# Kernel optimization log

Measured on AMD Instinct MI355X. Metric: run time of the kernel, lower is better.

## Reference

```python
import jax, jax.numpy as jnp
import numpy as np

B, C, T = 128, 23, 2000
N_FFT, HOP = 200, 100
NFREQ = N_FFT // 2 + 1        # 101
FT = 1 + (T - N_FFT) // HOP   # 19 time frames per channel
EMB, HEADS, DEPTH = 256, 8, 4
DH = EMB // HEADS             # 32 head dim
FF = 4 * EMB                  # 1024 ffn hidden
MASK_RATIO = 0.15


def _posenc(n, d):
    pos = np.arange(n)[:, None].astype(np.float32)
    div = np.exp(np.arange(0, d, 2).astype(np.float32) * -(np.log(10000.0) / d))
    pe = np.zeros((n, d), np.float32)
    pe[:, 0::2] = np.sin(pos * div)
    pe[:, 1::2] = np.cos(pos * div)
    return jnp.asarray(pe)


def _stft_mag(sig):
    # sig: (..., T) -> (..., FT, NFREQ); rectangular window, center=False, onesided
    idx = np.arange(FT)[:, None] * HOP + np.arange(N_FFT)[None, :]
    frames = sig[..., idx]                      # (..., FT, N_FFT)
    return jnp.abs(jnp.fft.rfft(frames, axis=-1))


def _layernorm(x, g, b):
    mu = x.mean(-1, keepdims=True)
    var = x.var(-1, keepdims=True)
    return (x - mu) / jnp.sqrt(var + 1e-5) * g + b


def setup_inputs() -> dict:
    key = jax.random.key(0)
    ks = jax.random.split(key, 12)
    inp = {
        'x': jax.random.normal(ks[0], (B, C, T), jnp.float32),
        'mask': jax.random.uniform(ks[1], (B, C, T)) < MASK_RATIO,
        'n_channel_offset': 0,
        'W_proj': jax.random.normal(ks[2], (NFREQ, EMB), jnp.float32) / np.sqrt(NFREQ),
        'b_proj': jnp.zeros((EMB,), jnp.float32),
        'channel_tokens': jax.random.normal(ks[3], (C, EMB), jnp.float32),
        'ln1_g': jnp.ones((DEPTH, EMB), jnp.float32),
        'ln1_b': jnp.zeros((DEPTH, EMB), jnp.float32),
        'Wq': jax.random.normal(ks[4], (DEPTH, EMB, EMB), jnp.float32) / np.sqrt(EMB),
        'Wk': jax.random.normal(ks[5], (DEPTH, EMB, EMB), jnp.float32) / np.sqrt(EMB),
        'Wv': jax.random.normal(ks[6], (DEPTH, EMB, EMB), jnp.float32) / np.sqrt(EMB),
        'Wo': jax.random.normal(ks[7], (DEPTH, EMB, EMB), jnp.float32) / np.sqrt(EMB),
        'ln2_g': jnp.ones((DEPTH, EMB), jnp.float32),
        'ln2_b': jnp.zeros((DEPTH, EMB), jnp.float32),
        'W1': jax.random.normal(ks[8], (DEPTH, EMB, FF), jnp.float32) / np.sqrt(EMB),
        'b1': jnp.zeros((DEPTH, FF), jnp.float32),
        'W2': jax.random.normal(ks[9], (DEPTH, FF, EMB), jnp.float32) / np.sqrt(FF),
        'b2': jnp.zeros((DEPTH, EMB), jnp.float32),
    }
    return inp


def reference(x, mask, n_channel_offset, W_proj, b_proj, channel_tokens,
              ln1_g, ln1_b, Wq, Wk, Wv, Wo, ln2_g, ln2_b, W1, b1, W2, b2):
    xm = jnp.where(mask, 0.0, x)
    # STFT magnitude for all channels at once: (B, C, FT, NFREQ)
    spec_c = _stft_mag(x)
    spec_m = _stft_mag(xm)
    # patch-frequency linear embedding -> (B, C, FT, EMB)
    emb_c = spec_c @ W_proj + b_proj
    emb_m = spec_m @ W_proj + b_proj
    tok = jnp.take(channel_tokens, jnp.arange(C) + n_channel_offset, axis=0)
    pe = _posenc(FT, EMB)
    emb_c = emb_c + tok[None, :, None, :] + pe[None, None, :, :]
    emb_m = emb_m + tok[None, :, None, :] + pe[None, None, :, :]
    S = C * FT
    emb_c = emb_c.reshape(B, S, EMB)
    h = emb_m.reshape(B, S, EMB)

    scale = DH ** -0.5
    for l in range(DEPTH):
        # linear attention block (prenorm)
        hn = _layernorm(h, ln1_g[l], ln1_b[l])
        q = (hn @ Wq[l]).reshape(B, S, HEADS, DH).transpose(0, 2, 1, 3)
        k = (hn @ Wk[l]).reshape(B, S, HEADS, DH).transpose(0, 2, 1, 3)
        v = (hn @ Wv[l]).reshape(B, S, HEADS, DH).transpose(0, 2, 1, 3)
        q = jax.nn.softmax(q, axis=-1) * scale   # softmax over feature dim
        k = jax.nn.softmax(k, axis=-2)           # softmax over sequence dim
        ctx = jnp.einsum('bhsd,bhse->bhde', k, v)      # (B,H,DH,DH)
        attn = jnp.einsum('bhsd,bhde->bhse', q, ctx)   # (B,H,S,DH)
        attn = attn.transpose(0, 2, 1, 3).reshape(B, S, EMB)
        h = h + attn @ Wo[l]
        # feed-forward block (prenorm)
        hn = _layernorm(h, ln2_g[l], ln2_b[l])
        h = h + jax.nn.gelu(hn @ W1[l] + b1[l]) @ W2[l] + b2[l]
    return (emb_c, h)
```

## Files before the change

kernel.cpp:

```cpp
#include <hip/hip_runtime.h>
#include <math.h>

#define BB 128
#define CC 23
#define TT 2000
#define NFFT 200
#define HOP 100
#define NFREQ 101
#define FTW 19
#define EMB 256
#define HEADS 8
#define DH 32
#define FFD 1024
#define DEPTH 4
#define SS (CC*FTW)
#define NROWS (BB*SS)
#define ROWT 16

typedef __attribute__((ext_vector_type(8))) short bf16x8;
typedef __attribute__((ext_vector_type(4))) float f32x4;
#define MFMA16 __builtin_amdgcn_mfma_f32_16x16x32_bf16

__device__ inline unsigned short f2bf(float f) {
    unsigned u = __float_as_uint(f);
    unsigned r = (u + 0x7FFFu + ((u >> 16) & 1u)) >> 16;
    return (unsigned short)r;
}
__device__ inline float bf2f(unsigned short s) {
    return __uint_as_float(((unsigned)s) << 16);
}
__device__ inline bf16x8 ld_frag(const unsigned short* p) {
    union { uint4 u; bf16x8 f; } v;
    v.u = *(const uint4*)p;
    return v.f;
}

__global__ __launch_bounds__(256) void k_init(float* pe) {
    int i = blockIdx.x * 256 + threadIdx.x;
    if (i < FTW * (EMB / 2)) {
        int t = i / (EMB / 2), j = i % (EMB / 2);
        float dv = expf((-9.210340371976184f / (float)EMB) * (float)(2 * j));
        float a = (float)t * dv;
        pe[t * EMB + 2 * j]     = sinf(a);
        pe[t * EMB + 2 * j + 1] = cosf(a);
    }
}

__global__ __launch_bounds__(256) void k_binit(unsigned short* Bt) {
    int i = blockIdx.x * 256 + threadIdx.x;
    if (i >= 256 * 224) return;
    int n = i / 224, k = i - (i / 224) * 224;
    int fq = ((n >> 5) << 4) + (n & 15);
    int kind = (n >> 4) & 1;
    float v = 0.f;
    if (k < 200 && fq < 101) {
        int kn = (fq * k) % 200;
        float th = 6.283185307179586f * (float)kn / 200.f;
        v = kind ? sinf(th) : cosf(th);
    }
    Bt[n * 224 + k] = f2bf(v);
}

__global__ __launch_bounds__(256) void k_tr(const float* __restrict__ in, unsigned short* __restrict__ out,
                                            int K, int N, size_t inStride, size_t outStride) {
    __shared__ float t[32][33];
    int k0 = blockIdx.y * 32, n0 = blockIdx.x * 32;
    const float* ip = in + blockIdx.z * inStride;
    unsigned short* op = out + blockIdx.z * outStride;
    int tx = threadIdx.x & 31, ty = threadIdx.x >> 5;
#pragma unroll
    for (int i = 0; i < 32; i += 8)
        t[ty + i][tx] = ip[(size_t)(k0 + ty + i) * N + n0 + tx];
    __syncthreads();
#pragma unroll
    for (int i = 0; i < 32; i += 8)
        op[(size_t)(n0 + ty + i) * K + k0 + tx] = f2bf(t[tx][ty + i]);
}

__global__ __launch_bounds__(256, 2) void k_stft(const float* __restrict__ x,
                                                 const int* __restrict__ mask,
                                                 const unsigned short* __restrict__ Bt,
                                                 float* __restrict__ specc,
                                                 float* __restrict__ specm) {
    int masked = blockIdx.y;
    int r0 = blockIdx.x * 64;
    __shared__ unsigned short aT[64 * 232];
    for (int t = threadIdx.x; t < 64 * 29; t += 256) {
        int row = t / 29;
        int ch = t - row * 29;
        int col0 = ch * 8;
        union { uint4 u; unsigned short s[8]; } pk;
        if (col0 < 200) {
            int fr = r0 + row;
            int bc = fr / 19, f = fr - bc * 19;
            const float* src = x + (size_t)bc * TT + f * HOP + col0;
            float4 v0 = *(const float4*)src;
            float4 v1 = *(const float4*)(src + 4);
            if (masked) {
                const int* ms = mask + (size_t)bc * TT + f * HOP + col0;
                int4 m0 = *(const int4*)ms;
                int4 m1 = *(const int4*)(ms + 4);
                if (m0.x) v0.x = 0.f; if (m0.y) v0.y = 0.f; if (m0.z) v0.z = 0.f; if (m0.w) v0.w = 0.f;
                if (m1.x) v1.x = 0.f; if (m1.y) v1.y = 0.f; if (m1.z) v1.z = 0.f; if (m1.w) v1.w = 0.f;
            }
            pk.s[0] = f2bf(v0.x); pk.s[1] = f2bf(v0.y); pk.s[2] = f2bf(v0.z); pk.s[3] = f2bf(v0.w);
            pk.s[4] = f2bf(v1.x); pk.s[5] = f2bf(v1.y); pk.s[6] = f2bf(v1.z); pk.s[7] = f2bf(v1.w);
        } else {
            pk.u = (uint4){0, 0, 0, 0};
        }
        *(uint4*)&aT[row * 232 + col0] = pk.u;
    }
    __syncthreads();
    int lane = threadIdx.x & 63, w = threadIdx.x >> 6;
    int m16 = lane & 15, q = lane >> 4;
    f32x4 acc[4][4];
#pragma unroll
    for (int mt = 0; mt < 4; mt++)
#pragma unroll
        for (int nt = 0; nt < 4; nt++) acc[mt][nt] = (f32x4){0.f, 0.f, 0.f, 0.f};
    for (int kk = 0; kk < 7; kk++) {
        int k0 = kk * 32 + q * 8;
        bf16x8 af[4], bfr[4];
#pragma unroll
        for (int mt = 0; mt < 4; mt++) af[mt] = ld_frag(&aT[(mt * 16 + m16) * 232 + k0]);
#pragma unroll
        for (int nt = 0; nt < 4; nt++) bfr[nt] = ld_frag(&Bt[(w * 64 + nt * 16 + m16) * 224 + k0]);
#pragma unroll
        for (int mt = 0; mt < 4; mt++)
#pragma unroll
            for (int nt = 0; nt < 4; nt++) acc[mt][nt] = MFMA16(af[mt], bfr[nt], acc[mt][nt], 0, 0, 0);
    }
    float* out = masked ? specm : specc;
#pragma unroll
    for (int pt = 0; pt < 2; pt++) {
        int fq = w * 32 + pt * 16 + m16;
        if (fq < NFREQ) {
#pragma unroll
            for (int mt = 0; mt < 4; mt++)
#pragma unroll
                for (int r = 0; r < 4; r++) {
                    float re = acc[mt][pt * 2][r];
                    float im = acc[mt][pt * 2 + 1][r];
                    int row = mt * 16 + q * 4 + r;
                    out[(size_t)(r0 + row) * NFREQ + fq] = sqrtf(re * re + im * im);
                }
        }
    }
}

__global__ __launch_bounds__(256) void k_proj(const float* __restrict__ spec,
                                              const float* __restrict__ Wp,
                                              const float* __restrict__ bp,
                                              const float* __restrict__ tok,
                                              const int* __restrict__ offp,
                                              const float* __restrict__ pe,
                                              float* __restrict__ out) {
    int r0 = blockIdx.x * ROWT;
    __shared__ float sp[ROWT][NFREQ];
    for (int i = threadIdx.x; i < ROWT * NFREQ; i += 256) {
        int r = i / NFREQ, kk = i % NFREQ;
        sp[r][kk] = spec[(size_t)(r0 + r) * NFREQ + kk];
    }
    __syncthreads();
    int j = threadIdx.x;
    float acc[ROWT];
#pragma unroll
    for (int r = 0; r < ROWT; r++) acc[r] = 0.f;
    for (int kk = 0; kk < NFREQ; kk++) {
        float w = Wp[kk * EMB + j];
#pragma unroll
        for (int r = 0; r < ROWT; r++) acc[r] += sp[r][kk] * w;
    }
    int off = *offp;
    float bj = bp[j];
#pragma unroll
    for (int r = 0; r < ROWT; r++) {
        int g = r0 + r;
        int c = (g / FTW) % CC;
        int f = g % FTW;
        out[(size_t)g * EMB + j] = acc[r] + bj + tok[(c + off) * EMB + j] + pe[f * EMB + j];
    }
}

__device__ inline void ln_stage(const float* __restrict__ h, int r0,
                                const float* __restrict__ g, const float* __restrict__ b,
                                unsigned short* aT) {
    int row = threadIdx.x >> 2, part = threadIdx.x & 3;
    const float* hr = h + (size_t)(r0 + row) * EMB + part * 64;
    float s1 = 0.f, s2 = 0.f;
#pragma unroll
    for (int i = 0; i < 16; i++) {
        float4 v = *(const float4*)(hr + i * 4);
        s1 += v.x + v.y + v.z + v.w;
        s2 += v.x * v.x + v.y * v.y + v.z * v.z + v.w * v.w;
    }
    s1 += __shfl_xor(s1, 1); s1 += __shfl_xor(s1, 2);
    s2 += __shfl_xor(s2, 1); s2 += __shfl_xor(s2, 2);
    float mu = s1 * (1.f / EMB);
    float var = s2 * (1.f / EMB) - mu * mu;
    float rstd = rsqrtf(var + 1e-5f);
#pragma unroll
    for (int i = 0; i < 8; i++) {
        int c0 = part * 64 + i * 8;
        float4 va = *(const float4*)(hr + i * 8);
        float4 vb = *(const float4*)(hr + i * 8 + 4);
        float4 ga = *(const float4*)(g + c0);
        float4 gb = *(const float4*)(g + c0 + 4);
        float4 ba = *(const float4*)(b + c0);
        float4 bb = *(const float4*)(b + c0 + 4);
        union { uint4 u; unsigned short s[8]; } pk;
        pk.s[0] = f2bf((va.x - mu) * rstd * ga.x + ba.x);
        pk.s[1] = f2bf((va.y - mu) * rstd * ga.y + ba.y);
        pk.s[2] = f2bf((va.z - mu) * rstd * ga.z + ba.z);
        pk.s[3] = f2bf((va.w - mu) * rstd * ga.w + ba.w);
        pk.s[4] = f2bf((vb.x - mu) * rstd * gb.x + bb.x);
        pk.s[5] = f2bf((vb.y - mu) * rstd * gb.y + bb.y);
        pk.s[6] = f2bf((vb.z - mu) * rstd * gb.z + bb.z);
        pk.s[7] = f2bf((vb.w - mu) * rstd * gb.w + bb.w);
        *(uint4*)&aT[row * 264 + c0] = pk.u;
    }
}

__global__ __launch_bounds__(256, 2) void k_qkv(const float* __restrict__ h,
                                                const float* __restrict__ lng,
                                                const float* __restrict__ lnb,
                                                const unsigned short* __restrict__ Wt,
                                                unsigned short* __restrict__ qb,
                                                unsigned short* __restrict__ kb,
                                                unsigned short* __restrict__ vb) {
    __shared__ unsigned short aT[64 * 264];
    __shared__ unsigned short ot[4][64 * 72];
    int r0 = blockIdx.x * 64;
    ln_stage(h, r0, lng, lnb, aT);
    __syncthreads();
    int lane = threadIdx.x & 63, w = threadIdx.x >> 6;
    int m16 = lane & 15, q = lane >> 4;
    for (int gg = 0; gg < 3; gg++) {
        int c0 = w * 192 + gg * 64;
        f32x4 acc[4][4];
#pragma unroll
        for (int mt = 0; mt < 4; mt++)
#pragma unroll
            for (int nt = 0; nt < 4; nt++) acc[mt][nt] = (f32x4){0.f, 0.f, 0.f, 0.f};
        for (int kk = 0; kk < 8; kk++) {
            int k0 = kk * 32 + q * 8;
            bf16x8 af[4], bfr[4];
#pragma unroll
            for (int mt = 0; mt < 4; mt++) af[mt] = ld_frag(&aT[(mt * 16 + m16) * 264 + k0]);
#pragma unroll
            for (int nt = 0; nt < 4; nt++) bfr[nt] = ld_frag(&Wt[(size_t)(c0 + nt * 16 + m16) * EMB + k0]);
#pragma unroll
            for (int mt = 0; mt < 4; mt++)
#pragma unroll
                for (int nt = 0; nt < 4; nt++) acc[mt][nt] = MFMA16(af[mt], bfr[nt], acc[mt][nt], 0, 0, 0);
        }
#pragma unroll
        for (int nt = 0; nt < 4; nt++)
#pragma unroll
            for (int mt = 0; mt < 4; mt++)
#pragma unroll
                for (int r = 0; r < 4; r++)
                    ot[w][(mt * 16 + q * 4 + r) * 72 + nt * 16 + m16] = f2bf(acc[mt][nt][r]);
        unsigned short* dst;
        int cc0;
        if (c0 < 256)      { dst = qb; cc0 = c0; }
        else if (c0 < 512) { dst = kb; cc0 = c0 - 256; }
        else               { dst = vb; cc0 = c0 - 512; }
        for (int t = lane; t < 512; t += 64) {
            int row = t >> 3, c8 = (t & 7) * 8;
            *(uint4*)&dst[(size_t)(r0 + row) * EMB + cc0 + c8] = *(uint4*)&ot[w][row * 72 + c8];
        }
    }
}

__global__ __launch_bounds__(256) void k_kctx(const unsigned short* __restrict__ kb,
                                              const unsigned short* __restrict__ vb,
                                              float* __restrict__ ctx) {
    int b = blockIdx.x >> 3, h = blockIdx.x & 7;
    int d = threadIdx.x & 31, g = threadIdx.x >> 5;
    size_t colbase = (size_t)b * SS * EMB + h * DH;
    __shared__ float red[8][32];
    __shared__ float kmax[32], krs[32];
    float mx = -1e30f;
    for (int s = g; s < SS; s += 8) mx = fmaxf(mx, bf2f(kb[colbase + (size_t)s * EMB + d]));
    red[g][d] = mx;
    __syncthreads();
    if (threadIdx.x < 32) {
        mx = red[0][d];
        for (int i = 1; i < 8; i++) mx = fmaxf(mx, red[i][d]);
        kmax[d] = mx;
    }
    __syncthreads();
    mx = kmax[d];
    float sm = 0.f;
    for (int s = g; s < SS; s += 8) sm += __expf(bf2f(kb[colbase + (size_t)s * EMB + d]) - mx);
    __syncthreads();
    red[g][d] = sm;
    __syncthreads();
    if (threadIdx.x < 32) {
        sm = 0.f;
        for (int i = 0; i < 8; i++) sm += red[i][d];
        krs[d] = 1.f / sm;
    }
    __syncthreads();
    int e = threadIdx.x & 31, db = threadIdx.x >> 5;
    float acc[4] = {0.f, 0.f, 0.f, 0.f};
    __shared__ float ksm[8][32], vls[8][32];
    float kmd = kmax[d], krd = krs[d];
    for (int s0 = 0; s0 < SS; s0 += 8) {
        int s = s0 + g;
        float kvv = 0.f, vvv = 0.f;
        if (s < SS) {
            kvv = __expf(bf2f(kb[colbase + (size_t)s * EMB + d]) - kmd) * krd;
            vvv = bf2f(vb[colbase + (size_t)s * EMB + d]);
        }
        __syncthreads();
        ksm[g][d] = kvv;
        vls[g][d] = vvv;
        __syncthreads();
#pragma unroll
        for (int ssx = 0; ssx < 8; ssx++) {
            float vv = vls[ssx][e];
#pragma unroll
            for (int i = 0; i < 4; i++) acc[i] += ksm[ssx][db * 4 + i] * vv;
        }
    }
#pragma unroll
    for (int i = 0; i < 4; i++)
        ctx[((size_t)b * HEADS + h) * 1024 + e * 32 + (db * 4 + i)] = acc[i];
}

__global__ __launch_bounds__(256, 4) void k_attn_o(const unsigned short* __restrict__ qb,
                                                   const float* __restrict__ ctxT,
                                                   const unsigned short* __restrict__ WoT,
                                                   float* __restrict__ h) {
    int b = blockIdx.x, s0 = blockIdx.y * 16;
    __shared__ unsigned short qsmb[16 * 264];
    __shared__ unsigned short ctxb[8 * 32 * 48];
    __shared__ unsigned short atb[16 * 264];
    int j = threadIdx.x;
    for (int idx = j; idx < 8192; idx += 256) {
        int hh = idx >> 10, rem = idx & 1023, e = rem >> 5, d = rem & 31;
        ctxb[hh * (32 * 48) + e * 48 + d] = f2bf(ctxT[(size_t)b * 8192 + idx]);
    }
    const float scale = 0.17677669529663687f;
    for (int r = 0; r < 16; r++) {
        int s = s0 + r; if (s > SS - 1) s = SS - 1;
        float v = bf2f(qb[((size_t)b * SS + s) * EMB + j]);
        float mxv = v;
#pragma unroll
        for (int m = 1; m < 32; m <<= 1) mxv = fmaxf(mxv, __shfl_xor(mxv, m));
        float ex = __expf(v - mxv);
        float sm = ex;
#pragma unroll
        for (int m = 1; m < 32; m <<= 1) sm += __shfl_xor(sm, m);
        qsmb[r * 264 + j] = f2bf(ex / sm * scale);
    }
    __syncthreads();
    int lane = threadIdx.x & 63, w = threadIdx.x >> 6;
    int m16 = lane & 15, q = lane >> 4;
#pragma unroll
    for (int hi = 0; hi < 2; hi++) {
        int head = w * 2 + hi;
        bf16x8 af = ld_frag(&qsmb[m16 * 264 + head * 32 + q * 8]);
#pragma unroll
        for (int half = 0; half < 2; half++) {
            bf16x8 bfr = ld_frag(&ctxb[head * (32 * 48) + (half * 16 + m16) * 48 + q * 8]);
            f32x4 acc = (f32x4){0.f, 0.f, 0.f, 0.f};
            acc = MFMA16(af, bfr, acc, 0, 0, 0);
#pragma unroll
            for (int r = 0; r < 4; r++)
                atb[(q * 4 + r) * 264 + head * 32 + half * 16 + m16] = f2bf(acc[r]);
        }
    }
    __syncthreads();
    f32x4 acc2[4];
#pragma unroll
    for (int nt = 0; nt < 4; nt++) acc2[nt] = (f32x4){0.f, 0.f, 0.f, 0.f};
    for (int kk = 0; kk < 8; kk++) {
        int k0 = kk * 32 + q * 8;
        bf16x8 af = ld_frag(&atb[m16 * 264 + k0]);
#pragma unroll
        for (int nt = 0; nt < 4; nt++) {
            bf16x8 bfr = ld_frag(&WoT[(size_t)(w * 64 + nt * 16 + m16) * EMB + k0]);
            acc2[nt] = MFMA16(af, bfr, acc2[nt], 0, 0, 0);
        }
    }
#pragma unroll
    for (int nt = 0; nt < 4; nt++) {
        int c = w * 64 + nt * 16 + m16;
#pragma unroll
        for (int r = 0; r < 4; r++) {
            int s = s0 + q * 4 + r;
            if (s < SS) h[((size_t)b * SS + s) * EMB + c] += acc2[nt][r];
        }
    }
}

__global__ __launch_bounds__(256, 2) void k_ffn(const float* __restrict__ hin,
                                                const float* __restrict__ lng,
                                                const float* __restrict__ lnb,
                                                const unsigned short* __restrict__ W1T,
                                                const float* __restrict__ b1,
                                                const unsigned short* __restrict__ W2T,
                                                const float* __restrict__ b2,
                                                float* __restrict__ h) {
    __shared__ unsigned short aT[64 * 264];
    __shared__ unsigned short fch[64 * 264];
    int r0 = blockIdx.x * 64;
    ln_stage(hin, r0, lng, lnb, aT);
    __syncthreads();
    int lane = threadIdx.x & 63, w = threadIdx.x >> 6;
    int m16 = lane & 15, q = lane >> 4;
    f32x4 acc2[4][4];
#pragma unroll
    for (int mt = 0; mt < 4; mt++)
#pragma unroll
        for (int nt = 0; nt < 4; nt++) acc2[mt][nt] = (f32x4){0.f, 0.f, 0.f, 0.f};
    for (int ch = 0; ch < 4; ch++) {
        f32x4 accf[4][4];
#pragma unroll
        for (int mt = 0; mt < 4; mt++)
#pragma unroll
            for (int nt = 0; nt < 4; nt++) accf[mt][nt] = (f32x4){0.f, 0.f, 0.f, 0.f};
        for (int kk = 0; kk < 8; kk++) {
            int k0 = kk * 32 + q * 8;
            bf16x8 af[4], bfr[4];
#pragma unroll
            for (int mt = 0; mt < 4; mt++) af[mt] = ld_frag(&aT[(mt * 16 + m16) * 264 + k0]);
#pragma unroll
            for (int nt = 0; nt < 4; nt++)
                bfr[nt] = ld_frag(&W1T[(size_t)(ch * 256 + w * 64 + nt * 16 + m16) * EMB + k0]);
#pragma unroll
            for (int mt = 0; mt < 4; mt++)
#pragma unroll
                for (int nt = 0; nt < 4; nt++) accf[mt][nt] = MFMA16(af[mt], bfr[nt], accf[mt][nt], 0, 0, 0);
        }
        __syncthreads();
#pragma unroll
        for (int nt = 0; nt < 4; nt++) {
            int cl = w * 64 + nt * 16 + m16;
            float bias = b1[ch * 256 + cl];
#pragma unroll
            for (int mt = 0; mt < 4; mt++)
#pragma unroll
                for (int r = 0; r < 4; r++) {
                    float xv = accf[mt][nt][r] + bias;
                    float z = 0.7978845608028654f * (xv + 0.044715f * xv * xv * xv);
                    z = fminf(fmaxf(z, -15.f), 15.f);
                    float t = __expf(2.f * z);
                    float gl = 0.5f * xv * (1.f + (t - 1.f) / (t + 1.f));
                    fch[(mt * 16 + q * 4 + r) * 264 + cl] = f2bf(gl);
                }
        }
        __syncthreads();
        for (int kk = 0; kk < 8; kk++) {
            int k0 = kk * 32 + q * 8;
            bf16x8 af[4], bfr[4];
#pragma unroll
            for (int mt = 0; mt < 4; mt++) af[mt] = ld_frag(&fch[(mt * 16 + m16) * 264 + k0]);
#pragma unroll
            for (int nt = 0; nt < 4; nt++)
                bfr[nt] = ld_frag(&W2T[(size_t)(w * 64 + nt * 16 + m16) * FFD + ch * 256 + k0]);
#pragma unroll
            for (int mt = 0; mt < 4; mt++)
#pragma unroll
                for (int nt = 0; nt < 4; nt++) acc2[mt][nt] = MFMA16(af[mt], bfr[nt], acc2[mt][nt], 0, 0, 0);
        }
    }
#pragma unroll
    for (int nt = 0; nt < 4; nt++) {
        int c = w * 64 + nt * 16 + m16;
        float bias = b2[c];
#pragma unroll
        for (int mt = 0; mt < 4; mt++)
#pragma unroll
            for (int r = 0; r < 4; r++)
                h[(size_t)(r0 + mt * 16 + q * 4 + r) * EMB + c] += acc2[mt][nt][r] + bias;
    }
}

extern "C" void kernel_launch(void* const* d_in, const int* in_sizes, int n_in,
                              void* d_out, int out_size, void* d_ws, size_t ws_size,
                              hipStream_t stream) {
    const float* x    = (const float*)d_in[0];
    const int* mask   = (const int*)d_in[1];
    const int* offp   = (const int*)d_in[2];
    const float* Wp   = (const float*)d_in[3];
    const float* bp   = (const float*)d_in[4];
    const float* tok  = (const float*)d_in[5];
    const float* ln1g = (const float*)d_in[6];
    const float* ln1b = (const float*)d_in[7];
    const float* Wq   = (const float*)d_in[8];
    const float* Wk   = (const float*)d_in[9];
    const float* Wv   = (const float*)d_in[10];
    const float* Wo   = (const float*)d_in[11];
    const float* ln2g = (const float*)d_in[12];
    const float* ln2b = (const float*)d_in[13];
    const float* W1   = (const float*)d_in[14];
    const float* b1   = (const float*)d_in[15];
    const float* W2   = (const float*)d_in[16];
    const float* b2   = (const float*)d_in[17];

    float* out_embc = (float*)d_out;
    float* h = out_embc + (size_t)NROWS * EMB;

    char* base = (char*)d_ws;
    float* pe = (float*)base;
    unsigned short* Bt = (unsigned short*)(base + 19712);
    unsigned short* wT = (unsigned short*)(base + 134400);
    unsigned short* qb = (unsigned short*)(base + 6425856);
    unsigned short* kb = qb + (size_t)NROWS * EMB;
    unsigned short* vb = kb + (size_t)NROWS * EMB;
    float* specc = (float*)qb;
    float* specm = specc + (size_t)NROWS * NFREQ;
    float* ctxT = (float*)(base + 6425856 + 3ull * NROWS * EMB * 2);

    unsigned short* WqkvT = wT;
    unsigned short* WoT   = wT + 786432;
    unsigned short* W1T   = WoT + 262144;
    unsigned short* W2T   = W1T + 1048576;

    k_init<<<10, 256, 0, stream>>>(pe);
    k_binit<<<224, 256, 0, stream>>>(Bt);
    k_tr<<<dim3(8, 8, 4), 256, 0, stream>>>(Wq, WqkvT + 0,      256, 256, 65536, 196608);
    k_tr<<<dim3(8, 8, 4), 256, 0, stream>>>(Wk, WqkvT + 65536,  256, 256, 65536, 196608);
    k_tr<<<dim3(8, 8, 4), 256, 0, stream>>>(Wv, WqkvT + 131072, 256, 256, 65536, 196608);
    k_tr<<<dim3(8, 8, 4), 256, 0, stream>>>(Wo, WoT, 256, 256, 65536, 65536);
    k_tr<<<dim3(32, 8, 4), 256, 0, stream>>>(W1, W1T, 256, 1024, 262144, 262144);
    k_tr<<<dim3(8, 32, 4), 256, 0, stream>>>(W2, W2T, 1024, 256, 262144, 262144);

    k_stft<<<dim3(NROWS / 64, 2), 256, 0, stream>>>(x, mask, Bt, specc, specm);
    k_proj<<<NROWS / ROWT, 256, 0, stream>>>(specc, Wp, bp, tok, offp, pe, out_embc);
    k_proj<<<NROWS / ROWT, 256, 0, stream>>>(specm, Wp, bp, tok, offp, pe, h);

    for (int l = 0; l < DEPTH; l++) {
        k_qkv<<<NROWS / 64, 256, 0, stream>>>(h, ln1g + l * EMB, ln1b + l * EMB,
                                              WqkvT + (size_t)l * 196608, qb, kb, vb);
        k_kctx<<<BB * HEADS, 256, 0, stream>>>(kb, vb, ctxT);
        k_attn_o<<<dim3(BB, (SS + 15) / 16), 256, 0, stream>>>(qb, ctxT, WoT + (size_t)l * 65536, h);
        k_ffn<<<NROWS / 64, 256, 0, stream>>>(h, ln2g + l * EMB, ln2b + l * EMB,
                                              W1T + (size_t)l * 262144, b1 + (size_t)l * FFD,
                                              W2T + (size_t)l * 262144, b2 + (size_t)l * EMB, h);
    }
}
```

Before: 2.389 ms.

## Use 512-thread blocks with register-prefetched weights in QKV and FFN kernels

The QKV and FFN kernels go from 4 to 8 waves per block, so each wave computes a 64x32 output tile instead of 64x64. Weight fragments are now prefetched one k-step ahead into registers. The QKV output is staged through one shared tile and written out cooperatively by the whole block, and layernorm is spread over 8 threads per row. The aim is more waves in flight to hide global weight-load latency and higher occupancy from smaller per-wave accumulators. The cost is more block-wide syncs and each A fragment being reused across only two N tiles.

```diff
diff --git a/kernel.cpp b/kernel.cpp
--- a/kernel.cpp
+++ b/kernel.cpp
@@ -182,32 +182,33 @@
     }
 }
 
-__device__ inline void ln_stage(const float* __restrict__ h, int r0,
-                                const float* __restrict__ g, const float* __restrict__ b,
-                                unsigned short* aT) {
-    int row = threadIdx.x >> 2, part = threadIdx.x & 3;
-    const float* hr = h + (size_t)(r0 + row) * EMB + part * 64;
+__device__ inline void ln_stage8(const float* __restrict__ h, int r0,
+                                 const float* __restrict__ g, const float* __restrict__ b,
+                                 unsigned short* aT) {
+    int row = threadIdx.x >> 3, part = threadIdx.x & 7;
+    const float* hr = h + (size_t)(r0 + row) * EMB + part * 32;
     float s1 = 0.f, s2 = 0.f;
 #pragma unroll
-    for (int i = 0; i < 16; i++) {
+    for (int i = 0; i < 8; i++) {
         float4 v = *(const float4*)(hr + i * 4);
         s1 += v.x + v.y + v.z + v.w;
         s2 += v.x * v.x + v.y * v.y + v.z * v.z + v.w * v.w;
     }
-    s1 += __shfl_xor(s1, 1); s1 += __shfl_xor(s1, 2);
-    s2 += __shfl_xor(s2, 1); s2 += __shfl_xor(s2, 2);
+    s1 += __shfl_xor(s1, 1); s1 += __shfl_xor(s1, 2); s1 += __shfl_xor(s1, 4);
+    s2 += __shfl_xor(s2, 1); s2 += __shfl_xor(s2, 2); s2 += __shfl_xor(s2, 4);
     float mu = s1 * (1.f / EMB);
     float var = s2 * (1.f / EMB) - mu * mu;
     float rstd = rsqrtf(var + 1e-5f);
-#pragma unroll
-    for (int i = 0; i < 8; i++) {
-        int c0 = part * 64 + i * 8;
+    const float* gp = g + part * 32;
+    const float* bp = b + part * 32;
+#pragma unroll
+    for (int i = 0; i < 4; i++) {
         float4 va = *(const float4*)(hr + i * 8);
         float4 vb = *(const float4*)(hr + i * 8 + 4);
-        float4 ga = *(const float4*)(g + c0);
-        float4 gb = *(const float4*)(g + c0 + 4);
-        float4 ba = *(const float4*)(b + c0);
-        float4 bb = *(const float4*)(b + c0 + 4);
+        float4 ga = *(const float4*)(gp + i * 8);
+        float4 gb = *(const float4*)(gp + i * 8 + 4);
+        float4 ba = *(const float4*)(bp + i * 8);
+        float4 bb = *(const float4*)(bp + i * 8 + 4);
         union { uint4 u; unsigned short s[8]; } pk;
         pk.s[0] = f2bf((va.x - mu) * rstd * ga.x + ba.x);
         pk.s[1] = f2bf((va.y - mu) * rstd * ga.y + ba.y);
@@ -217,11 +218,11 @@
         pk.s[5] = f2bf((vb.y - mu) * rstd * gb.y + bb.y);
         pk.s[6] = f2bf((vb.z - mu) * rstd * gb.z + bb.z);
         pk.s[7] = f2bf((vb.w - mu) * rstd * gb.w + bb.w);
-        *(uint4*)&aT[row * 264 + c0] = pk.u;
-    }
-}
-
-__global__ __launch_bounds__(256, 2) void k_qkv(const float* __restrict__ h,
+        *(uint4*)&aT[row * 264 + part * 32 + i * 8] = pk.u;
+    }
+}
+
+__global__ __launch_bounds__(512, 4) void k_qkv(const float* __restrict__ h,
                                                 const float* __restrict__ lng,
                                                 const float* __restrict__ lnb,
                                                 const unsigned short* __restrict__ Wt,
@@ -229,47 +230,57 @@
                                                 unsigned short* __restrict__ kb,
                                                 unsigned short* __restrict__ vb) {
     __shared__ unsigned short aT[64 * 264];
-    __shared__ unsigned short ot[4][64 * 72];
+    __shared__ unsigned short ob[64 * 264];
     int r0 = blockIdx.x * 64;
-    ln_stage(h, r0, lng, lnb, aT);
+    ln_stage8(h, r0, lng, lnb, aT);
     __syncthreads();
     int lane = threadIdx.x & 63, w = threadIdx.x >> 6;
     int m16 = lane & 15, q = lane >> 4;
-    for (int gg = 0; gg < 3; gg++) {
-        int c0 = w * 192 + gg * 64;
-        f32x4 acc[4][4];
+    f32x4 acc[4][2];
+
+    auto do_gemm = [&](int gg) {
+        int cb = gg * 256 + w * 32;
 #pragma unroll
         for (int mt = 0; mt < 4; mt++)
 #pragma unroll
-            for (int nt = 0; nt < 4; nt++) acc[mt][nt] = (f32x4){0.f, 0.f, 0.f, 0.f};
+            for (int nt = 0; nt < 2; nt++) acc[mt][nt] = (f32x4){0.f, 0.f, 0.f, 0.f};
+        bf16x8 bc0 = ld_frag(&Wt[(size_t)(cb + m16) * EMB + q * 8]);
+        bf16x8 bc1 = ld_frag(&Wt[(size_t)(cb + 16 + m16) * EMB + q * 8]);
         for (int kk = 0; kk < 8; kk++) {
             int k0 = kk * 32 + q * 8;
-            bf16x8 af[4], bfr[4];
+            bf16x8 bn0, bn1;
+            if (kk < 7) {
+                bn0 = ld_frag(&Wt[(size_t)(cb + m16) * EMB + k0 + 32]);
+                bn1 = ld_frag(&Wt[(size_t)(cb + 16 + m16) * EMB + k0 + 32]);
+            }
+            bf16x8 af[4];
 #pragma unroll
             for (int mt = 0; mt < 4; mt++) af[mt] = ld_frag(&aT[(mt * 16 + m16) * 264 + k0]);
 #pragma unroll
-            for (int nt = 0; nt < 4; nt++) bfr[nt] = ld_frag(&Wt[(size_t)(c0 + nt * 16 + m16) * EMB + k0]);
+            for (int mt = 0; mt < 4; mt++) acc[mt][0] = MFMA16(af[mt], bc0, acc[mt][0], 0, 0, 0);
+#pragma unroll
+            for (int mt = 0; mt < 4; mt++) acc[mt][1] = MFMA16(af[mt], bc1, acc[mt][1], 0, 0, 0);
+            bc0 = bn0; bc1 = bn1;
+        }
+    };
+
+    do_gemm(0);
+    for (int gg = 0; gg < 3; gg++) {
+        __syncthreads();
+#pragma unroll
+        for (int nt = 0; nt < 2; nt++)
 #pragma unroll
             for (int mt = 0; mt < 4; mt++)
 #pragma unroll
-                for (int nt = 0; nt < 4; nt++) acc[mt][nt] = MFMA16(af[mt], bfr[nt], acc[mt][nt], 0, 0, 0);
-        }
-#pragma unroll
-        for (int nt = 0; nt < 4; nt++)
-#pragma unroll
-            for (int mt = 0; mt < 4; mt++)
-#pragma unroll
                 for (int r = 0; r < 4; r++)
-                    ot[w][(mt * 16 + q * 4 + r) * 72 + nt * 16 + m16] = f2bf(acc[mt][nt][r]);
-        unsigned short* dst;
-        int cc0;
-        if (c0 < 256)      { dst = qb; cc0 = c0; }
-        else if (c0 < 512) { dst = kb; cc0 = c0 - 256; }
-        else               { dst = vb; cc0 = c0 - 512; }
-        for (int t = lane; t < 512; t += 64) {
-            int row = t >> 3, c8 = (t & 7) * 8;
-            *(uint4*)&dst[(size_t)(r0 + row) * EMB + cc0 + c8] = *(uint4*)&ot[w][row * 72 + c8];
-        }
+                    ob[(mt * 16 + q * 4 + r) * 264 + w * 32 + nt * 16 + m16] = f2bf(acc[mt][nt][r]);
+        __syncthreads();
+        unsigned short* dst = (gg == 0) ? qb : (gg == 1) ? kb : vb;
+        for (int t = threadIdx.x; t < 2048; t += 512) {
+            int row = t >> 5, c8 = (t & 31) * 8;
+            *(uint4*)&dst[(size_t)(r0 + row) * EMB + c8] = *(uint4*)&ob[row * 264 + c8];
+        }
+        if (gg < 2) do_gemm(gg + 1);
     }
 }
 
@@ -397,7 +408,7 @@
     }
 }
 
-__global__ __launch_bounds__(256, 2) void k_ffn(const float* __restrict__ hin,
+__global__ __launch_bounds__(512, 4) void k_ffn(const float* __restrict__ hin,
                                                 const float* __restrict__ lng,
                                                 const float* __restrict__ lnb,
                                                 const unsigned short* __restrict__ W1T,
@@ -408,38 +419,49 @@
     __shared__ unsigned short aT[64 * 264];
     __shared__ unsigned short fch[64 * 264];
     int r0 = blockIdx.x * 64;
-    ln_stage(hin, r0, lng, lnb, aT);
+    ln_stage8(hin, r0, lng, lnb, aT);
     __syncthreads();
     int lane = threadIdx.x & 63, w = threadIdx.x >> 6;
     int m16 = lane & 15, q = lane >> 4;
-    f32x4 acc2[4][4];
+    f32x4 acc2[4][2];
 #pragma unroll
     for (int mt = 0; mt < 4; mt++)
 #pragma unroll
-        for (int nt = 0; nt < 4; nt++) acc2[mt][nt] = (f32x4){0.f, 0.f, 0.f, 0.f};
-    for (int ch = 0; ch < 4; ch++) {
-        f32x4 accf[4][4];
+        for (int nt = 0; nt < 2; nt++) acc2[mt][nt] = (f32x4){0.f, 0.f, 0.f, 0.f};
+    f32x4 accf[4][2];
+
+    auto gemm1 = [&](int ch) {
+        int cb = ch * 256 + w * 32;
 #pragma unroll
         for (int mt = 0; mt < 4; mt++)
 #pragma unroll
-            for (int nt = 0; nt < 4; nt++) accf[mt][nt] = (f32x4){0.f, 0.f, 0.f, 0.f};
+            for (int nt = 0; nt < 2; nt++) accf[mt][nt] = (f32x4){0.f, 0.f, 0.f, 0.f};
+        bf16x8 bc0 = ld_frag(&W1T[(size_t)(cb + m16) * EMB + q * 8]);
+        bf16x8 bc1 = ld_frag(&W1T[(size_t)(cb + 16 + m16) * EMB + q * 8]);
         for (int kk = 0; kk < 8; kk++) {
             int k0 = kk * 32 + q * 8;
-            bf16x8 af[4], bfr[4];
+            bf16x8 bn0, bn1;
+            if (kk < 7) {
+                bn0 = ld_frag(&W1T[(size_t)(cb + m16) * EMB + k0 + 32]);
+                bn1 = ld_frag(&W1T[(size_t)(cb + 16 + m16) * EMB + k0 + 32]);
+            }
+            bf16x8 af[4];
 #pragma unroll
             for (int mt = 0; mt < 4; mt++) af[mt] = ld_frag(&aT[(mt * 16 + m16) * 264 + k0]);
 #pragma unroll
-            for (int nt = 0; nt < 4; nt++)
-                bfr[nt] = ld_frag(&W1T[(size_t)(ch * 256 + w * 64 + nt * 16 + m16) * EMB + k0]);
-#pragma unroll
-            for (int mt = 0; mt < 4; mt++)
-#pragma unroll
-                for (int nt = 0; nt < 4; nt++) accf[mt][nt] = MFMA16(af[mt], bfr[nt], accf[mt][nt], 0, 0, 0);
-        }
+            for (int mt = 0; mt < 4; mt++) accf[mt][0] = MFMA16(af[mt], bc0, accf[mt][0], 0, 0, 0);
+#pragma unroll
+            for (int mt = 0; mt < 4; mt++) accf[mt][1] = MFMA16(af[mt], bc1, accf[mt][1], 0, 0, 0);
+            bc0 = bn0; bc1 = bn1;
+        }
+    };
+
+    gemm1(0);
+    for (int ch = 0; ch < 4; ch++) {
         __syncthreads();
 #pragma unroll
-        for (int nt = 0; nt < 4; nt++) {
-            int cl = w * 64 + nt * 16 + m16;
+        for (int nt = 0; nt < 2; nt++) {
+            int cl = w * 32 + nt * 16 + m16;
             float bias = b1[ch * 256 + cl];
 #pragma unroll
             for (int mt = 0; mt < 4; mt++)
@@ -454,23 +476,32 @@
                 }
         }
         __syncthreads();
-        for (int kk = 0; kk < 8; kk++) {
-            int k0 = kk * 32 + q * 8;
-            bf16x8 af[4], bfr[4];
-#pragma unroll
-            for (int mt = 0; mt < 4; mt++) af[mt] = ld_frag(&fch[(mt * 16 + m16) * 264 + k0]);
-#pragma unroll
-            for (int nt = 0; nt < 4; nt++)
-                bfr[nt] = ld_frag(&W2T[(size_t)(w * 64 + nt * 16 + m16) * FFD + ch * 256 + k0]);
-#pragma unroll
-            for (int mt = 0; mt < 4; mt++)
-#pragma unroll
-                for (int nt = 0; nt < 4; nt++) acc2[mt][nt] = MFMA16(af[mt], bfr[nt], acc2[mt][nt], 0, 0, 0);
-        }
-    }
-#pragma unroll
-    for (int nt = 0; nt < 4; nt++) {
-        int c = w * 64 + nt * 16 + m16;
+        {
+            int rb = w * 32;
+            bf16x8 bc0 = ld_frag(&W2T[(size_t)(rb + m16) * FFD + ch * 256 + q * 8]);
+            bf16x8 bc1 = ld_frag(&W2T[(size_t)(rb + 16 + m16) * FFD + ch * 256 + q * 8]);
+            for (int kk = 0; kk < 8; kk++) {
+                int k0 = kk * 32 + q * 8;
+                bf16x8 bn0, bn1;
+                if (kk < 7) {
+                    bn0 = ld_frag(&W2T[(size_t)(rb + m16) * FFD + ch * 256 + k0 + 32]);
+                    bn1 = ld_frag(&W2T[(size_t)(rb + 16 + m16) * FFD + ch * 256 + k0 + 32]);
+                }
+                bf16x8 af[4];
+#pragma unroll
+                for (int mt = 0; mt < 4; mt++) af[mt] = ld_frag(&fch[(mt * 16 + m16) * 264 + k0]);
+#pragma unroll
+                for (int mt = 0; mt < 4; mt++) acc2[mt][0] = MFMA16(af[mt], bc0, acc2[mt][0], 0, 0, 0);
+#pragma unroll
+                for (int mt = 0; mt < 4; mt++) acc2[mt][1] = MFMA16(af[mt], bc1, acc2[mt][1], 0, 0, 0);
+                bc0 = bn0; bc1 = bn1;
+            }
+        }
+        if (ch < 3) gemm1(ch + 1);
+    }
+#pragma unroll
+    for (int nt = 0; nt < 2; nt++) {
+        int c = w * 32 + nt * 16 + m16;
         float bias = b2[c];
 #pragma unroll
         for (int mt = 0; mt < 4; mt++)
@@ -535,11 +566,11 @@
     k_proj<<<NROWS / ROWT, 256, 0, stream>>>(specm, Wp, bp, tok, offp, pe, h);
 
     for (int l = 0; l < DEPTH; l++) {
-        k_qkv<<<NROWS / 64, 256, 0, stream>>>(h, ln1g + l * EMB, ln1b + l * EMB,
+        k_qkv<<<NROWS / 64, 512, 0, stream>>>(h, ln1g + l * EMB, ln1b + l * EMB,
                                               WqkvT + (size_t)l * 196608, qb, kb, vb);
         k_kctx<<<BB * HEADS, 256, 0, stream>>>(kb, vb, ctxT);
         k_attn_o<<<dim3(BB, (SS + 15) / 16), 256, 0, stream>>>(qb, ctxT, WoT + (size_t)l * 65536, h);
-        k_ffn<<<NROWS / 64, 256, 0, stream>>>(h, ln2g + l * EMB, ln2b + l * EMB,
+        k_ffn<<<NROWS / 64, 512, 0, stream>>>(h, ln2g + l * EMB, ln2b + l * EMB,
                                               W1T + (size_t)l * 262144, b1 + (size_t)l * FFD,
                                               W2T + (size_t)l * 262144, b2 + (size_t)l * EMB, h);
     }
```

New measurement: 2.153 ms. 9.9% less time.
